# Performance work log

Measured on AMD Instinct MI355X. Metric: run time of the kernel, lower is better.

## Reference

```python
import jax, jax.numpy as jnp
import numpy as np

D = 32          # embedding_size
B = 16384       # batch_size
P = 16          # neighbor_sample_size (paths per item per hop)
NE = 100000     # n_entity
NU = 100000     # n_user
NR = 32         # n_relation
N_ITER = 2


def setup_inputs() -> dict:
    key = jax.random.key(0)
    ks = jax.random.split(key, 20)
    s = 0.1
    nrm = lambda k, sh: jax.random.normal(k, sh, dtype=jnp.float32) * s
    inp = {
        "user_table": nrm(ks[0], (NU, D)),
        "ent_table": nrm(ks[1], (NE, D)),
        "rel_table": nrm(ks[2], (NR, D)),
        # PyTorch LSTM params, gate order (i, f, g, o)
        "w_ih0": nrm(ks[3], (4 * D, 2 * D)),
        "w_hh0": nrm(ks[4], (4 * D, D)),
        "b_ih0": nrm(ks[5], (4 * D,)),
        "b_hh0": nrm(ks[6], (4 * D,)),
        "w_ih1": nrm(ks[7], (4 * D, 2 * D)),
        "w_hh1": nrm(ks[8], (4 * D, D)),
        "b_ih1": nrm(ks[9], (4 * D,)),
        "b_hh1": nrm(ks[10], (4 * D,)),
        "agg_w": nrm(ks[11], (D, D)),
        "agg_b": nrm(ks[12], (D,)),
        "users": jax.random.randint(ks[13], (B,), 0, NU),
        "items": jax.random.randint(ks[14], (B,), 0, NE),
        "ratings": jax.random.randint(ks[15], (B,), 0, 2),
        # hop h path table: [n_entity, P, 2*(h+1)+1]; values < 32 valid for both tables
        "lp0": jax.random.randint(ks[16], (NE, P, 3), 0, 32),
        "lp1": jax.random.randint(ks[17], (NE, P, 5), 0, 32),
    }
    return inp


def _lstm_last(seq, w_ih, w_hh, b_ih, b_hh):
    # seq: [N, T, 2D] -> final hidden state [N, D], PyTorch gate order i,f,g,o
    N = seq.shape[0]
    H = w_hh.shape[1]
    bias = b_ih + b_hh

    def step(carry, x):
        h, c = carry
        g = x @ w_ih.T + h @ w_hh.T + bias
        i, f, gg, o = jnp.split(g, 4, axis=-1)
        c = jax.nn.sigmoid(f) * c + jax.nn.sigmoid(i) * jnp.tanh(gg)
        h = jax.nn.sigmoid(o) * jnp.tanh(c)
        return (h, c), None

    h0 = jnp.zeros((N, H), seq.dtype)
    (h, _), _ = jax.lax.scan(step, (h0, h0), jnp.swapaxes(seq, 0, 1))
    return h


def _forward(user_table, ent_table, rel_table, lstm_params, agg_w, agg_b,
             users, items, ratings, lps):
    u = user_table[users]                # [B, D]
    items_emb = ent_table[items]         # [B, D]
    for hop in range(N_ITER):
        lp = lps[hop]
        w_ih, w_hh, b_ih, b_hh = lstm_params[hop]
        il = lp[items]                   # [B, P, 2*(hop+1)+1]
        seed_e = ent_table[il[:, :, 0]]  # [B, P, D]
        u_b = jnp.broadcast_to(u[:, None, :], seed_e.shape)
        first = jnp.concatenate([u_b, seed_e], -1)[:, :, None, :]   # [B,P,1,2D]
        rel_e = rel_table[il[:, :, 1::2]]                            # [B,P,hop+1,D]
        tail_e = ent_table[il[:, :, 2::2]]                           # [B,P,hop+1,D]
        rest = jnp.concatenate([rel_e, tail_e], -1)                  # [B,P,hop+1,2D]
        seq = jnp.concatenate([first, rest], 2).reshape(B * P, hop + 2, 2 * D)
        h = _lstm_last(seq, w_ih, w_hh, b_ih, b_hh)                  # [B*P, D]
        final = h.reshape(B, P, D).sum(axis=1)                       # hidden_out sum
        items_emb = (items_emb + final) @ agg_w.T + agg_b            # 'sum' aggregator
    scores = jnp.sum(u * items_emb, axis=-1)                         # [B]
    r = ratings.astype(scores.dtype)
    # stable BCE on sigmoid(scores)
    loss = -jnp.mean(r * jax.nn.log_sigmoid(scores) + (1.0 - r) * jax.nn.log_sigmoid(-scores))
    return loss, jax.nn.sigmoid(scores)


def reference(user_table, ent_table, rel_table,
              w_ih0, w_hh0, b_ih0, b_hh0,
              w_ih1, w_hh1, b_ih1, b_hh1,
              agg_w, agg_b,
              users, items, ratings, lp0, lp1):
    lstm_params = [(w_ih0, w_hh0, b_ih0, b_hh0), (w_ih1, w_hh1, b_ih1, b_hh1)]
    loss, scores_normalized = _forward(user_table, ent_table, rel_table,
                                       lstm_params, agg_w, agg_b,
                                       users, items, ratings, (lp0, lp1))
    return (loss, scores_normalized, items)
```

## Files before the change

### kernel.cpp

```cpp
#include <hip/hip_runtime.h>
#include <math.h>

#define D  32
#define BN 16384
#define PP 16

typedef __bf16 bf16x8 __attribute__((ext_vector_type(8)));
typedef __bf16 bf16x4 __attribute__((ext_vector_type(4)));
typedef float  floatx4 __attribute__((ext_vector_type(4)));

#define K1 1.44269504088896341f
#define K2 2.88539008177792681f

#define WU_OFF     0
#define WHH_OFF    10240
#define WIMG_BYTES 20480
#define H_OFF      20480
#define LDS_BYTES  (WIMG_BYTES + 4 * 1280)

__device__ __forceinline__ float sigf(float x) {
    float e = __builtin_amdgcn_exp2f(-x * K1);
    return __builtin_amdgcn_rcpf(1.0f + e);
}
__device__ __forceinline__ float logsigf(float x) {
    float ax = fabsf(x);
    float l = log1pf(__expf(-ax));
    return (x >= 0.0f) ? -l : x - l;
}
__device__ __forceinline__ bf16x8 loadu8(const float* __restrict__ p) {
    float4 a = ((const float4*)p)[0], b = ((const float4*)p)[1];
    bf16x8 r = { (__bf16)a.x, (__bf16)a.y, (__bf16)a.z, (__bf16)a.w,
                 (__bf16)b.x, (__bf16)b.y, (__bf16)b.z, (__bf16)b.w };
    return r;
}

__global__ __launch_bounds__(256)
void prep_tables(const float* __restrict__ ent, const float* __restrict__ rel,
                 const float* __restrict__ wih0, const float* __restrict__ whh0,
                 const float* __restrict__ bih0, const float* __restrict__ bhh0,
                 const float* __restrict__ wih1, const float* __restrict__ whh1,
                 const float* __restrict__ bih1, const float* __restrict__ bhh1,
                 float* __restrict__ T0, float* __restrict__ T,
                 float* __restrict__ wimg)
{
    const int id = blockIdx.x * 256 + threadIdx.x;
    if (id < 16384) {
        const int hop  = id >> 13;
        const int rest = id & 8191;
        const int mat  = rest >> 12;
        const int e    = rest & 4095;
        const int gate = e >> 5, d = e & 31;
        float v = mat ? (hop ? whh1 : whh0)[(size_t)gate * 32 + d]
                      : (hop ? wih1 : wih0)[(size_t)gate * 64 + d];
        __bf16* base = (__bf16*)((char*)wimg + hop * WIMG_BYTES + mat * 10240);
        base[gate * 40 + d] = (__bf16)v;
    } else if (id < 16384 + 262144) {
        const int idt = id - 16384;
        const int hop = idt >> 17;
        const int r   = idt & 131071;
        const int j   = r >> 12;
        const int k   = (r >> 7) & 31;
        const int g   = r & 127;
        const float* wih = hop ? wih1 : wih0;
        const float4* w4 = (const float4*)(wih + (size_t)g * 64);
        const float4* r4 = (const float4*)(rel + (size_t)j * 32);
        const float4* e4 = (const float4*)(ent + (size_t)k * 32);
        float a = hop ? bih1[g] + bhh1[g] : bih0[g] + bhh0[g];
        #pragma unroll
        for (int i = 0; i < 8; ++i) {
            float4 w = w4[i], x = r4[i];
            a = fmaf(w.x, x.x, a); a = fmaf(w.y, x.y, a);
            a = fmaf(w.z, x.z, a); a = fmaf(w.w, x.w, a);
        }
        #pragma unroll
        for (int i = 0; i < 8; ++i) {
            float4 w = w4[8 + i], x = e4[i];
            a = fmaf(w.x, x.x, a); a = fmaf(w.y, x.y, a);
            a = fmaf(w.z, x.z, a); a = fmaf(w.w, x.w, a);
        }
        T[(size_t)hop * 131072 + r] = a;
    } else if (id < 16384 + 262144 + 8192) {
        const int idb = id - 16384 - 262144;
        const int hop = idb >> 12;
        const int k   = (idb >> 7) & 31;
        const int g   = idb & 127;
        const float* wih = hop ? wih1 : wih0;
        const float4* w4 = (const float4*)(wih + (size_t)g * 64);
        const float4* e4 = (const float4*)(ent + (size_t)k * 32);
        float a = hop ? bih1[g] + bhh1[g] : bih0[g] + bhh0[g];
        #pragma unroll
        for (int i = 0; i < 8; ++i) {
            float4 w = w4[8 + i], x = e4[i];
            a = fmaf(w.x, x.x, a); a = fmaf(w.y, x.y, a);
            a = fmaf(w.z, x.z, a); a = fmaf(w.w, x.w, a);
        }
        T0[(size_t)hop * 4096 + k * 128 + g] = a;
    }
}

template<bool FIRST, bool LAST>
__device__ __forceinline__ void nonlin(
    floatx4* __restrict__ acc, float* __restrict__ cst,
    float* __restrict__ hlo, float* __restrict__ hhi,
    char* __restrict__ Hw, int q, int bnl)
{
    #pragma unroll
    for (int hf = 0; hf < 2; ++hf) {
        float* hout = hf ? hhi : hlo;
        #pragma unroll
        for (int r = 0; r < 4; ++r) {
            float gi = acc[0 + hf][r], gf = acc[2 + hf][r],
                  gg = acc[4 + hf][r], go = acc[6 + hf][r];
            float Ai = 1.0f + __builtin_amdgcn_exp2f(-gi * K1);
            float Af = 1.0f + __builtin_amdgcn_exp2f(-gf * K1);
            float G2 = __builtin_amdgcn_exp2f(gg * K2);
            float Gp = G2 + 1.0f, Gm = G2 - 1.0f;
            float cold = FIRST ? 0.0f : cst[hf * 4 + r];
            float num = cold * Ai * Gp + Gm * Af;
            float c = num * __builtin_amdgcn_rcpf(Af * Ai * Gp);
            cst[hf * 4 + r] = c;
            float Ao = 1.0f + __builtin_amdgcn_exp2f(-go * K1);
            float C2 = __builtin_amdgcn_exp2f(c * K2);
            hout[r] = (C2 - 1.0f) * __builtin_amdgcn_rcpf(Ao * (C2 + 1.0f));
        }
    }
    if (!LAST) {
        bf16x4 plo = { (__bf16)hlo[0], (__bf16)hlo[1], (__bf16)hlo[2], (__bf16)hlo[3] };
        bf16x4 phi = { (__bf16)hhi[0], (__bf16)hhi[1], (__bf16)hhi[2], (__bf16)hhi[3] };
        *(bf16x4*)(Hw + bnl * 80 + 8 * q)      = plo;
        *(bf16x4*)(Hw + bnl * 80 + 32 + 8 * q) = phi;
    }
}

__global__ __launch_bounds__(256, 4)
void hop_mfma(const float* __restrict__ user_table,
              const int*   __restrict__ users,
              const int*   __restrict__ items,
              const int*   __restrict__ lp0,
              const int*   __restrict__ lp1,
              const float* __restrict__ wimg,
              const float* __restrict__ T0g,
              const float* __restrict__ Tg,
              float* __restrict__ F0,
              float* __restrict__ F1)
{
    __shared__ __align__(16) char lds[LDS_BYTES];

    const bool second = blockIdx.x & 1;
    const int  idx    = blockIdx.x >> 1;
    const int tid  = threadIdx.x;
    const int lane = tid & 63;
    const int wave = tid >> 6;
    const int q    = lane >> 4;
    const int bnl  = lane & 15;

    const int fb = idx * 4 + wave;
    const int L  = second ? 5 : 3;
    const int* lp = second ? lp1 : lp0;
    const int* __restrict__ il = lp + ((size_t)items[fb] * PP + bnl) * L;
    int sq[5];
    #pragma unroll
    for (int i = 0; i < 5; ++i) sq[i] = (i < L) ? il[i] : 0;

    const float* T0h = T0g + (second ? 4096 : 0);
    const float* Th  = Tg  + (second ? 131072 : 0);
    const float* t0p = T0h + sq[0] * 128 + 4 * q;
    const float* t1p = Th + (((sq[1]) << 5) + sq[2]) * 128 + 4 * q;

    floatx4 acc0[8], acc1[8];
    #pragma unroll
    for (int mt = 0; mt < 8; ++mt) acc0[mt] = *(const floatx4*)(t0p + 16 * mt);
    #pragma unroll
    for (int mt = 0; mt < 8; ++mt) acc1[mt] = *(const floatx4*)(t1p + 16 * mt);

    bf16x8 bu = loadu8(user_table + (size_t)users[fb] * D + q * 8);

    {
        const float4* g4 = (const float4*)((const char*)wimg +
                                           (second ? WIMG_BYTES : 0));
        float4* l4 = (float4*)lds;
        #pragma unroll
        for (int i = 0; i < 5; ++i) l4[i * 256 + tid] = g4[i * 256 + tid];
    }
    const char* Wu  = lds + WU_OFF;
    const char* Whh = lds + WHH_OFF;
    char* Hw = lds + H_OFF + wave * 1280;

    __syncthreads();

    float cst[8], hlo[4], hhi[4];

    #pragma unroll
    for (int mt = 0; mt < 8; ++mt) {
        bf16x8 wu = *(const bf16x8*)(Wu + (16 * mt + bnl) * 80 + q * 16);
        acc0[mt] = __builtin_amdgcn_mfma_f32_16x16x32_bf16(wu, bu, acc0[mt], 0, 0, 0);
    }
    nonlin<true, false>(acc0, cst, hlo, hhi, Hw, q, bnl);

    floatx4 acc2[8];
    if (second) {
        const float* t2p = Th + (((sq[3]) << 5) + sq[4]) * 128 + 4 * q;
        #pragma unroll
        for (int mt = 0; mt < 8; ++mt) acc2[mt] = *(const floatx4*)(t2p + 16 * mt);
    }

    {
        bf16x8 bh = *(const bf16x8*)(Hw + bnl * 80 + q * 16);
        #pragma unroll
        for (int mt = 0; mt < 8; ++mt) {
            bf16x8 wh = *(const bf16x8*)(Whh + (16 * mt + bnl) * 80 + q * 16);
            acc1[mt] = __builtin_amdgcn_mfma_f32_16x16x32_bf16(wh, bh, acc1[mt], 0, 0, 0);
        }
        if (second) nonlin<false, false>(acc1, cst, hlo, hhi, Hw, q, bnl);
        else        nonlin<false, true >(acc1, cst, hlo, hhi, Hw, q, bnl);
    }

    if (second) {
        bf16x8 bh = *(const bf16x8*)(Hw + bnl * 80 + q * 16);
        #pragma unroll
        for (int mt = 0; mt < 8; ++mt) {
            bf16x8 wh = *(const bf16x8*)(Whh + (16 * mt + bnl) * 80 + q * 16);
            acc2[mt] = __builtin_amdgcn_mfma_f32_16x16x32_bf16(wh, bh, acc2[mt], 0, 0, 0);
        }
        nonlin<false, true>(acc2, cst, hlo, hhi, Hw, q, bnl);
    }

    #pragma unroll
    for (int r = 0; r < 4; ++r) {
        #pragma unroll
        for (int m = 1; m < 16; m <<= 1) {
            hlo[r] += __shfl_xor(hlo[r], m);
            hhi[r] += __shfl_xor(hhi[r], m);
        }
    }
    if (bnl == 0) {
        float* Fout = (second ? F1 : F0);
        float4 vlo = { hlo[0], hlo[1], hlo[2], hlo[3] };
        float4 vhi = { hhi[0], hhi[1], hhi[2], hhi[3] };
        *(float4*)(Fout + (size_t)fb * D + 4 * q)      = vlo;
        *(float4*)(Fout + (size_t)fb * D + 16 + 4 * q) = vhi;
    }
}

__global__ __launch_bounds__(256)
void chain_score(const float* __restrict__ user_table,
                 const float* __restrict__ ent_table,
                 const float* __restrict__ agg_w,
                 const float* __restrict__ agg_b,
                 const int*   __restrict__ users,
                 const int*   __restrict__ items,
                 const int*   __restrict__ ratings,
                 const float* __restrict__ F0,
                 const float* __restrict__ F1,
                 float* __restrict__ out,
                 float* __restrict__ partials)
{
    __shared__ float s[8][33];
    __shared__ float red[8];
    const int tid = threadIdx.x;
    const int bb  = tid >> 5;
    const int j   = tid & 31;
    const int b   = blockIdx.x * 8 + bb;
    const int it  = items[b];

    s[bb][j] = ent_table[(size_t)it * D + j] + F0[(size_t)b * D + j];
    __syncthreads();
    const float* __restrict__ w = agg_w + (size_t)j * D;
    float e0 = agg_b[j];
    #pragma unroll
    for (int k = 0; k < D; ++k) e0 = fmaf(s[bb][k], w[k], e0);
    __syncthreads();
    s[bb][j] = e0 + F1[(size_t)b * D + j];
    __syncthreads();
    float e1 = agg_b[j];
    #pragma unroll
    for (int k = 0; k < D; ++k) e1 = fmaf(s[bb][k], w[k], e1);

    float prod = user_table[(size_t)users[b] * D + j] * e1;
    #pragma unroll
    for (int m = 1; m < 32; m <<= 1) prod += __shfl_xor(prod, m);
    if (j == 0) {
        out[1 + b]      = sigf(prod);
        out[1 + BN + b] = (float)it;
        float r = (float)ratings[b];
        red[bb] = r * logsigf(prod) + (1.0f - r) * logsigf(-prod);
    }
    __syncthreads();
    if (tid == 0) {
        float t = 0.0f;
        #pragma unroll
        for (int qq = 0; qq < 8; ++qq) t += red[qq];
        partials[blockIdx.x] = t;
    }
}

__global__ __launch_bounds__(256)
void loss_kernel(const float* __restrict__ partials, float* __restrict__ out)
{
    __shared__ float red[4];
    const int t = threadIdx.x;
    float v = 0.0f;
    #pragma unroll
    for (int qq = 0; qq < 8; ++qq) v += partials[qq * 256 + t];
    #pragma unroll
    for (int m = 1; m < 64; m <<= 1) v += __shfl_xor(v, m);
    if ((t & 63) == 0) red[t >> 6] = v;
    __syncthreads();
    if (t == 0) out[0] = -(red[0] + red[1] + red[2] + red[3]) / (float)BN;
}

extern "C" void kernel_launch(void* const* d_in, const int* in_sizes, int n_in,
                              void* d_out, int out_size, void* d_ws, size_t ws_size,
                              hipStream_t stream)
{
    const float* user_table = (const float*)d_in[0];
    const float* ent_table  = (const float*)d_in[1];
    const float* rel_table  = (const float*)d_in[2];
    const float* w_ih0 = (const float*)d_in[3];
    const float* w_hh0 = (const float*)d_in[4];
    const float* b_ih0 = (const float*)d_in[5];
    const float* b_hh0 = (const float*)d_in[6];
    const float* w_ih1 = (const float*)d_in[7];
    const float* w_hh1 = (const float*)d_in[8];
    const float* b_ih1 = (const float*)d_in[9];
    const float* b_hh1 = (const float*)d_in[10];
    const float* agg_w = (const float*)d_in[11];
    const float* agg_b = (const float*)d_in[12];
    const int* users   = (const int*)d_in[13];
    const int* items   = (const int*)d_in[14];
    const int* ratings = (const int*)d_in[15];
    const int* lp0     = (const int*)d_in[16];
    const int* lp1     = (const int*)d_in[17];
    float* out = (float*)d_out;

    float* ws       = (float*)d_ws;
    float* F0       = ws;
    float* F1       = F0 + (size_t)BN * D;
    float* partials = F1 + (size_t)BN * D;
    float* T0       = partials + 2048;
    float* T        = T0 + 8192;
    float* wimg     = T + 262144;

    prep_tables<<<1120, 256, 0, stream>>>(ent_table, rel_table,
        w_ih0, w_hh0, b_ih0, b_hh0, w_ih1, w_hh1, b_ih1, b_hh1, T0, T, wimg);
    hop_mfma<<<8192, 256, 0, stream>>>(
        user_table, users, items, lp0, lp1, wimg, T0, T, F0, F1);
    chain_score<<<BN / 8, 256, 0, stream>>>(
        user_table, ent_table, agg_w, agg_b, users, items, ratings,
        F0, F1, out, partials);
    loss_kernel<<<1, 256, 0, stream>>>(partials, out);
}
```

Measured before the change: 272.4 us.

## Split relation/entity gate tables and pre-pack path indices in prep kernel

Replaces the 32x32 combined relation-entity gate table with separate per-relation and per-entity tables that are summed in registers. This shrinks the precompute work and the table footprint. The prep kernel now also gathers the item path indices into packed byte-offset int4 records, so the hop kernel does one coalesced load instead of a dependent items→lp gather, and the table loads are issued earlier to overlap with MFMA and nonlinearity work. The final loss kernel launch is removed in favour of atomicAdd into an output zeroed in prep, which adds atomics and makes the sum order nondeterministic.

```diff
diff --git a/kernel.cpp b/kernel.cpp
--- a/kernel.cpp
+++ b/kernel.cpp
@@ -40,8 +40,11 @@
                  const float* __restrict__ bih0, const float* __restrict__ bhh0,
                  const float* __restrict__ wih1, const float* __restrict__ whh1,
                  const float* __restrict__ bih1, const float* __restrict__ bhh1,
-                 float* __restrict__ T0, float* __restrict__ T,
-                 float* __restrict__ wimg)
+                 const int* __restrict__ items,
+                 const int* __restrict__ lp0, const int* __restrict__ lp1,
+                 float* __restrict__ T0, float* __restrict__ TR,
+                 float* __restrict__ wimg, int* __restrict__ pidx,
+                 float* __restrict__ out)
 {
     const int id = blockIdx.x * 256 + threadIdx.x;
     if (id < 16384) {
@@ -54,47 +57,61 @@
                       : (hop ? wih1 : wih0)[(size_t)gate * 64 + d];
         __bf16* base = (__bf16*)((char*)wimg + hop * WIMG_BYTES + mat * 10240);
         base[gate * 40 + d] = (__bf16)v;
-    } else if (id < 16384 + 262144) {
-        const int idt = id - 16384;
-        const int hop = idt >> 17;
-        const int r   = idt & 131071;
-        const int j   = r >> 12;
-        const int k   = (r >> 7) & 31;
-        const int g   = r & 127;
+    } else if (id < 24576) {
+        const int idb = id - 16384;
+        const int hop = idb >> 12;
+        const int k   = (idb >> 7) & 31;
+        const int g   = idb & 127;
+        const float* wih = hop ? wih1 : wih0;
+        const float4* w4 = (const float4*)(wih + (size_t)g * 64 + 32);
+        const float4* e4 = (const float4*)(ent + (size_t)k * 32);
+        float a = hop ? bih1[g] + bhh1[g] : bih0[g] + bhh0[g];
+        #pragma unroll
+        for (int i = 0; i < 8; ++i) {
+            float4 w = w4[i], x = e4[i];
+            a = fmaf(w.x, x.x, a); a = fmaf(w.y, x.y, a);
+            a = fmaf(w.z, x.z, a); a = fmaf(w.w, x.w, a);
+        }
+        T0[hop * 4096 + k * 128 + g] = a;
+    } else if (id < 32768) {
+        const int idb = id - 24576;
+        const int hop = idb >> 12;
+        const int j   = (idb >> 7) & 31;
+        const int g   = idb & 127;
         const float* wih = hop ? wih1 : wih0;
         const float4* w4 = (const float4*)(wih + (size_t)g * 64);
         const float4* r4 = (const float4*)(rel + (size_t)j * 32);
-        const float4* e4 = (const float4*)(ent + (size_t)k * 32);
-        float a = hop ? bih1[g] + bhh1[g] : bih0[g] + bhh0[g];
+        float a = 0.0f;
         #pragma unroll
         for (int i = 0; i < 8; ++i) {
             float4 w = w4[i], x = r4[i];
             a = fmaf(w.x, x.x, a); a = fmaf(w.y, x.y, a);
             a = fmaf(w.z, x.z, a); a = fmaf(w.w, x.w, a);
         }
-        #pragma unroll
-        for (int i = 0; i < 8; ++i) {
-            float4 w = w4[8 + i], x = e4[i];
-            a = fmaf(w.x, x.x, a); a = fmaf(w.y, x.y, a);
-            a = fmaf(w.z, x.z, a); a = fmaf(w.w, x.w, a);
-        }
-        T[(size_t)hop * 131072 + r] = a;
-    } else if (id < 16384 + 262144 + 8192) {
-        const int idb = id - 16384 - 262144;
-        const int hop = idb >> 12;
-        const int k   = (idb >> 7) & 31;
-        const int g   = idb & 127;
-        const float* wih = hop ? wih1 : wih0;
-        const float4* w4 = (const float4*)(wih + (size_t)g * 64);
-        const float4* e4 = (const float4*)(ent + (size_t)k * 32);
-        float a = hop ? bih1[g] + bhh1[g] : bih0[g] + bhh0[g];
-        #pragma unroll
-        for (int i = 0; i < 8; ++i) {
-            float4 w = w4[8 + i], x = e4[i];
-            a = fmaf(w.x, x.x, a); a = fmaf(w.y, x.y, a);
-            a = fmaf(w.z, x.z, a); a = fmaf(w.w, x.w, a);
-        }
-        T0[(size_t)hop * 4096 + k * 128 + g] = a;
+        TR[hop * 4096 + j * 128 + g] = a;
+    } else if (id < 32768 + 524288) {
+        const int c   = id - 32768;
+        const int hop = c >> 18;
+        const int rem = c & 262143;
+        const int fb  = rem >> 4;
+        const int p   = rem & 15;
+        const int item = items[fb];
+        const int hb = hop << 14;
+        int w0, w1, w2 = 0;
+        if (hop == 0) {
+            const int* il = lp0 + ((size_t)item * PP + p) * 3;
+            w0 = hb + (il[0] << 9);
+            w1 = (hb + (il[1] << 9)) | ((hb + (il[2] << 9)) << 16);
+        } else {
+            const int* il = lp1 + ((size_t)item * PP + p) * 5;
+            w0 = hb + (il[0] << 9);
+            w1 = (hb + (il[1] << 9)) | ((hb + (il[2] << 9)) << 16);
+            w2 = (hb + (il[3] << 9)) | ((hb + (il[4] << 9)) << 16);
+        }
+        int4 v = { w0, w1, w2, 0 };
+        *(int4*)(pidx + ((size_t)(hop * BN + fb) * PP + p) * 4) = v;
+    } else if (id == 32768 + 524288) {
+        out[0] = 0.0f;
     }
 }
 
@@ -135,12 +152,10 @@
 __global__ __launch_bounds__(256, 4)
 void hop_mfma(const float* __restrict__ user_table,
               const int*   __restrict__ users,
-              const int*   __restrict__ items,
-              const int*   __restrict__ lp0,
-              const int*   __restrict__ lp1,
+              const int*   __restrict__ pidx,
               const float* __restrict__ wimg,
               const float* __restrict__ T0g,
-              const float* __restrict__ Tg,
+              const float* __restrict__ TRg,
               float* __restrict__ F0,
               float* __restrict__ F1)
 {
@@ -154,27 +169,6 @@
     const int q    = lane >> 4;
     const int bnl  = lane & 15;
 
-    const int fb = idx * 4 + wave;
-    const int L  = second ? 5 : 3;
-    const int* lp = second ? lp1 : lp0;
-    const int* __restrict__ il = lp + ((size_t)items[fb] * PP + bnl) * L;
-    int sq[5];
-    #pragma unroll
-    for (int i = 0; i < 5; ++i) sq[i] = (i < L) ? il[i] : 0;
-
-    const float* T0h = T0g + (second ? 4096 : 0);
-    const float* Th  = Tg  + (second ? 131072 : 0);
-    const float* t0p = T0h + sq[0] * 128 + 4 * q;
-    const float* t1p = Th + (((sq[1]) << 5) + sq[2]) * 128 + 4 * q;
-
-    floatx4 acc0[8], acc1[8];
-    #pragma unroll
-    for (int mt = 0; mt < 8; ++mt) acc0[mt] = *(const floatx4*)(t0p + 16 * mt);
-    #pragma unroll
-    for (int mt = 0; mt < 8; ++mt) acc1[mt] = *(const floatx4*)(t1p + 16 * mt);
-
-    bf16x8 bu = loadu8(user_table + (size_t)users[fb] * D + q * 8);
-
     {
         const float4* g4 = (const float4*)((const char*)wimg +
                                            (second ? WIMG_BYTES : 0));
@@ -182,6 +176,21 @@
         #pragma unroll
         for (int i = 0; i < 5; ++i) l4[i * 256 + tid] = g4[i * 256 + tid];
     }
+
+    const int fb = idx * 4 + wave;
+    const int4 ix = *(const int4*)(pidx +
+        ((size_t)((second ? BN : 0) + fb) * PP + bnl) * 4);
+
+    bf16x8 bu = loadu8(user_table + (size_t)users[fb] * D + q * 8);
+
+    const char* T0b = (const char*)T0g;
+    const char* TRb = (const char*)TRg;
+
+    const float* t0p = (const float*)(T0b + ix.x) + 4 * q;
+    floatx4 acc0[8];
+    #pragma unroll
+    for (int mt = 0; mt < 8; ++mt) acc0[mt] = *(const floatx4*)(t0p + 16 * mt);
+
     const char* Wu  = lds + WU_OFF;
     const char* Whh = lds + WHH_OFF;
     char* Hw = lds + H_OFF + wave * 1280;
@@ -195,15 +204,21 @@
         bf16x8 wu = *(const bf16x8*)(Wu + (16 * mt + bnl) * 80 + q * 16);
         acc0[mt] = __builtin_amdgcn_mfma_f32_16x16x32_bf16(wu, bu, acc0[mt], 0, 0, 0);
     }
+
+    const float* trp1 = (const float*)(TRb + (ix.y & 0xffff)) + 4 * q;
+    const float* tep1 = (const float*)(T0b + (((unsigned)ix.y) >> 16)) + 4 * q;
+    floatx4 tr1[8], te1[8];
+    #pragma unroll
+    for (int mt = 0; mt < 8; ++mt) {
+        tr1[mt] = *(const floatx4*)(trp1 + 16 * mt);
+        te1[mt] = *(const floatx4*)(tep1 + 16 * mt);
+    }
+
     nonlin<true, false>(acc0, cst, hlo, hhi, Hw, q, bnl);
 
-    floatx4 acc2[8];
-    if (second) {
-        const float* t2p = Th + (((sq[3]) << 5) + sq[4]) * 128 + 4 * q;
-        #pragma unroll
-        for (int mt = 0; mt < 8; ++mt) acc2[mt] = *(const floatx4*)(t2p + 16 * mt);
-    }
-
+    floatx4 acc1[8];
+    #pragma unroll
+    for (int mt = 0; mt < 8; ++mt) acc1[mt] = tr1[mt] + te1[mt];
     {
         bf16x8 bh = *(const bf16x8*)(Hw + bnl * 80 + q * 16);
         #pragma unroll
@@ -211,11 +226,26 @@
             bf16x8 wh = *(const bf16x8*)(Whh + (16 * mt + bnl) * 80 + q * 16);
             acc1[mt] = __builtin_amdgcn_mfma_f32_16x16x32_bf16(wh, bh, acc1[mt], 0, 0, 0);
         }
-        if (second) nonlin<false, false>(acc1, cst, hlo, hhi, Hw, q, bnl);
-        else        nonlin<false, true >(acc1, cst, hlo, hhi, Hw, q, bnl);
-    }
-
+    }
+
+    floatx4 tr2[8], te2[8];
     if (second) {
+        const float* trp2 = (const float*)(TRb + (ix.z & 0xffff)) + 4 * q;
+        const float* tep2 = (const float*)(T0b + (((unsigned)ix.z) >> 16)) + 4 * q;
+        #pragma unroll
+        for (int mt = 0; mt < 8; ++mt) {
+            tr2[mt] = *(const floatx4*)(trp2 + 16 * mt);
+            te2[mt] = *(const floatx4*)(tep2 + 16 * mt);
+        }
+    }
+
+    if (second) nonlin<false, false>(acc1, cst, hlo, hhi, Hw, q, bnl);
+    else        nonlin<false, true >(acc1, cst, hlo, hhi, Hw, q, bnl);
+
+    if (second) {
+        floatx4 acc2[8];
+        #pragma unroll
+        for (int mt = 0; mt < 8; ++mt) acc2[mt] = tr2[mt] + te2[mt];
         bf16x8 bh = *(const bf16x8*)(Hw + bnl * 80 + q * 16);
         #pragma unroll
         for (int mt = 0; mt < 8; ++mt) {
@@ -252,8 +282,7 @@
                  const int*   __restrict__ ratings,
                  const float* __restrict__ F0,
                  const float* __restrict__ F1,
-                 float* __restrict__ out,
-                 float* __restrict__ partials)
+                 float* __restrict__ out)
 {
     __shared__ float s[8][33];
     __shared__ float red[8];
@@ -290,23 +319,8 @@
         float t = 0.0f;
         #pragma unroll
         for (int qq = 0; qq < 8; ++qq) t += red[qq];
-        partials[blockIdx.x] = t;
-    }
-}
-
-__global__ __launch_bounds__(256)
-void loss_kernel(const float* __restrict__ partials, float* __restrict__ out)
-{
-    __shared__ float red[4];
-    const int t = threadIdx.x;
-    float v = 0.0f;
-    #pragma unroll
-    for (int qq = 0; qq < 8; ++qq) v += partials[qq * 256 + t];
-    #pragma unroll
-    for (int m = 1; m < 64; m <<= 1) v += __shfl_xor(v, m);
-    if ((t & 63) == 0) red[t >> 6] = v;
-    __syncthreads();
-    if (t == 0) out[0] = -(red[0] + red[1] + red[2] + red[3]) / (float)BN;
+        atomicAdd(out, -t / (float)BN);
+    }
 }
 
 extern "C" void kernel_launch(void* const* d_in, const int* in_sizes, int n_in,
@@ -333,20 +347,20 @@
     const int* lp1     = (const int*)d_in[17];
     float* out = (float*)d_out;
 
-    float* ws       = (float*)d_ws;
-    float* F0       = ws;
-    float* F1       = F0 + (size_t)BN * D;
-    float* partials = F1 + (size_t)BN * D;
-    float* T0       = partials + 2048;
-    float* T        = T0 + 8192;
-    float* wimg     = T + 262144;
-
-    prep_tables<<<1120, 256, 0, stream>>>(ent_table, rel_table,
-        w_ih0, w_hh0, b_ih0, b_hh0, w_ih1, w_hh1, b_ih1, b_hh1, T0, T, wimg);
+    float* ws   = (float*)d_ws;
+    float* F0   = ws;
+    float* F1   = F0 + (size_t)BN * D;
+    float* T0   = F1 + (size_t)BN * D;
+    float* TR   = T0 + 8192;
+    float* wimg = TR + 8192;
+    int*   pidx = (int*)(wimg + 10240);
+
+    prep_tables<<<2177, 256, 0, stream>>>(ent_table, rel_table,
+        w_ih0, w_hh0, b_ih0, b_hh0, w_ih1, w_hh1, b_ih1, b_hh1,
+        items, lp0, lp1, T0, TR, wimg, pidx, out);
     hop_mfma<<<8192, 256, 0, stream>>>(
-        user_table, users, items, lp0, lp1, wimg, T0, T, F0, F1);
+        user_table, users, pidx, wimg, T0, TR, F0, F1);
     chain_score<<<BN / 8, 256, 0, stream>>>(
         user_table, ent_table, agg_w, agg_b, users, items, ratings,
-        F0, F1, out, partials);
-    loss_kernel<<<1, 256, 0, stream>>>(partials, out);
-}
+        F0, F1, out);
+}
```

New measurement: 318.3 us. 16.8% more time.
